# Kernel tuning notes

Measured on AMD Instinct MI355X. Metric: run time of the kernel, lower is better.

## Reference

```python
import jax, jax.numpy as jnp
import numpy as np
from jax import lax

V, T, E, H = 50000, 32, 256, 512
B, S = 64, 512


def setup_inputs() -> dict:
    key = jax.random.key(0)
    ks = jax.random.split(key, 16)
    u = lambda k, shp, s=0.05: jax.random.uniform(k, shp, jnp.float32, -s, s)
    inp = {
        'emb': jax.random.normal(ks[0], (V, E), jnp.float32) * 0.1,
        'w_ih_f': u(ks[1], (4 * H, E)), 'w_hh_f': u(ks[2], (4 * H, H)), 'b_f': u(ks[3], (4 * H,)),
        'w_ih_b': u(ks[4], (4 * H, E)), 'w_hh_b': u(ks[5], (4 * H, H)), 'b_b': u(ks[6], (4 * H,)),
        'fc_w': u(ks[7], (T, 2 * H)), 'fc_b': u(ks[8], (T,)),
        'start_trans': u(ks[9], (T,), 0.1), 'end_trans': u(ks[10], (T,), 0.1),
        'trans': u(ks[11], (T, T), 0.1),
        'x': jax.random.randint(ks[12], (B, S), 0, V),
        'tags': jax.random.randint(ks[13], (B, S), 0, T),
    }
    return inp


def _lstm_dir(xp, w_hh, reverse):
    # xp: [S, B, 4H] precomputed input projections (+ combined bias)
    b, h4 = xp.shape[1], xp.shape[2]
    h_dim = h4 // 4
    h0 = jnp.zeros((b, h_dim), xp.dtype)
    c0 = jnp.zeros((b, h_dim), xp.dtype)

    def step(carry, xt):
        h, c = carry
        gates = xt + h @ w_hh.T
        i, f, g, o = jnp.split(gates, 4, axis=-1)
        i, f, o = jax.nn.sigmoid(i), jax.nn.sigmoid(f), jax.nn.sigmoid(o)
        c = f * c + i * jnp.tanh(g)
        h = o * jnp.tanh(c)
        return (h, c), h

    _, hs = lax.scan(step, (h0, c0), xp, reverse=reverse)
    return hs  # [S, B, H]


def reference(emb, w_ih_f, w_hh_f, b_f, w_ih_b, w_hh_b, b_b, fc_w, fc_b,
              start_trans, end_trans, trans, x, tags):
    # Embedding -> [S, B, E] (time-major for the scan)
    e = jnp.transpose(emb[x], (1, 0, 2))
    # One big GEMM per direction for input projections
    xp_f = jnp.einsum('sbe,ge->sbg', e, w_ih_f) + b_f
    xp_b = jnp.einsum('sbe,ge->sbg', e, w_ih_b) + b_b
    h_f = _lstm_dir(xp_f, w_hh_f, reverse=False)
    h_b = _lstm_dir(xp_b, w_hh_b, reverse=True)
    h = jnp.concatenate([h_f, h_b], axis=-1)          # [S, B, 2H]
    em = jnp.einsum('sbh,th->sbt', h, fc_w) + fc_b     # [S, B, T] emissions

    tags_t = tags.T                                    # [S, B]
    # CRF numerator: gold path score (mask = all ones)
    emit = jnp.take_along_axis(em, tags_t[:, :, None], axis=2)[..., 0]  # [S, B]
    tr = trans[tags_t[:-1], tags_t[1:]]                                  # [S-1, B]
    num = start_trans[tags_t[0]] + emit.sum(0) + tr.sum(0) + end_trans[tags_t[-1]]

    # CRF denominator: forward algorithm (log partition)
    alpha0 = start_trans[None, :] + em[0]              # [B, T]

    def step(alpha, et):
        # alpha: [B, T_prev]; et: [B, T_next]
        nxt = jax.nn.logsumexp(alpha[:, :, None] + trans[None, :, :] + et[:, None, :], axis=1)
        return nxt, None

    alpha, _ = lax.scan(step, alpha0, em[1:])
    den = jax.nn.logsumexp(alpha + end_trans[None, :], axis=1)  # [B]

    llh = num - den
    return -jnp.mean(llh)
```

## Files before the change

### kernel.cpp

```cpp
#include <hip/hip_runtime.h>
#include <hip/hip_bf16.h>
#include <cstdint>
#include <cstddef>


typedef __attribute__((ext_vector_type(8))) short short8;
typedef __attribute__((ext_vector_type(4))) float f32x4;

__device__ __forceinline__ unsigned short f2b(float x){
  unsigned u = __float_as_uint(x);
  unsigned r = u + 0x7FFFu + ((u >> 16) & 1u);
  return (unsigned short)(r >> 16);
}
__device__ __forceinline__ float b2f(unsigned short b){
  return __uint_as_float(((unsigned)b) << 16);
}
__device__ __forceinline__ float sigf(float x){
  return 1.f / (1.f + __expf(-x));
}
__device__ __forceinline__ float tanhfast(float x){
  return 1.f - 2.f / (__expf(2.f * x) + 1.f);
}


__global__ void prep_wc_kernel(const float* __restrict__ w_ih, const float* __restrict__ w_hh,
                               unsigned short* __restrict__ wc){
  int idx = blockIdx.x * 256 + threadIdx.x;
  if(idx >= 2048 * 768) return;
  int g = idx / 768, k = idx - g * 768;
  float v = (k < 256) ? w_ih[g * 256 + k] : w_hh[g * 512 + (k - 256)];
  wc[idx] = f2b(v);
}

__global__ void prep_fcw_kernel(const float* __restrict__ fc_w, unsigned short* __restrict__ fcwN){
  int idx = blockIdx.x * 256 + threadIdx.x;
  fcwN[idx] = f2b(fc_w[idx]);
}

__global__ void gather_kernel(const float* __restrict__ emb, const int* __restrict__ x,
                              unsigned short* __restrict__ e_bf){
  int tok = blockIdx.x;
  int s = tok >> 6, b = tok & 63;
  int row = x[b * 512 + s];
  int k = threadIdx.x;
  e_bf[(size_t)tok * 256 + k] = f2b(emb[(size_t)row * 256 + k]);
}

__global__ void init_cnt_kernel(unsigned int* __restrict__ cnt){
  int idx = blockIdx.x * 256 + threadIdx.x;
  if(idx < 1024) cnt[idx] = 0;
}

__global__ __launch_bounds__(256, 1) void lstm_persist(
    const unsigned short* __restrict__ e_bf,
    const unsigned short* __restrict__ Wc_f, const unsigned short* __restrict__ Wc_b,
    const float* __restrict__ b_f, const float* __restrict__ b_b,
    unsigned short* __restrict__ st_f, unsigned short* __restrict__ st_b,
    unsigned int* __restrict__ cnt)
{
  __shared__ float gate_lds[64 * 34];

  const int tid  = threadIdx.x;
  const int wid  = tid >> 6;
  const int lane = tid & 63;
  const int dir  = blockIdx.x >> 6;
  const int slice= blockIdx.x & 63;
  const int j0   = slice * 8;

  const int mh = wid >> 1;
  const int nh = wid & 1;
  const int r0 = lane & 15;
  const int kb = (lane >> 4) * 8;

  const unsigned short* Wc   = dir ? Wc_b : Wc_f;
  const float*          bias = dir ? b_b  : b_f;
  unsigned short*       st   = dir ? st_b : st_f;
  unsigned int*         cbase= cnt + dir * 512;

  const int c = nh * 16 + r0;
  const unsigned short* wrow = Wc + (size_t)((c >> 3) * 512 + j0 + (c & 7)) * 768;
  short8 bfrag[24];
#pragma unroll
  for(int kc = 0; kc < 24; kc++)
    bfrag[kc] = *(const short8*)(wrow + kc * 32 + kb);

  const int eb = tid >> 2, jp = tid & 3;
  const float bi0 = bias[0 * 512 + j0 + 2 * jp], bi1 = bias[0 * 512 + j0 + 2 * jp + 1];
  const float bf0 = bias[1 * 512 + j0 + 2 * jp], bf1 = bias[1 * 512 + j0 + 2 * jp + 1];
  const float bg0 = bias[2 * 512 + j0 + 2 * jp], bg1 = bias[2 * 512 + j0 + 2 * jp + 1];
  const float bo0 = bias[3 * 512 + j0 + 2 * jp], bo1 = bias[3 * 512 + j0 + 2 * jp + 1];
  float cc0 = 0.f, cc1 = 0.f;

  unsigned int* st32 = (unsigned int*)st;
  const unsigned long long* stq = (const unsigned long long*)st;
  const int arow0 = mh * 32 + r0;
  const int arow1 = arow0 + 16;

  union U { unsigned long long q[2]; short8 v; };

  for(int t = 0; t < 512; t++){
    const int t_e = dir ? (511 - t) : t;

    const unsigned short* ep0 = e_bf + (size_t)t_e * 16384 + (size_t)arow0 * 256;
    const unsigned short* ep1 = e_bf + (size_t)t_e * 16384 + (size_t)arow1 * 256;
    short8 ef0[8], ef1[8];
#pragma unroll
    for(int kc = 0; kc < 8; kc++){
      ef0[kc] = *(const short8*)(ep0 + kc * 32 + kb);
      ef1[kc] = *(const short8*)(ep1 + kc * 32 + kb);
    }
    f32x4 aE0 = {0,0,0,0}, aO0 = {0,0,0,0};
    f32x4 aE1 = {0,0,0,0}, aO1 = {0,0,0,0};
#pragma unroll
    for(int kc = 0; kc < 8; kc += 2){
      aE0 = __builtin_amdgcn_mfma_f32_16x16x32_bf16(ef0[kc],   bfrag[kc],   aE0, 0,0,0);
      aE1 = __builtin_amdgcn_mfma_f32_16x16x32_bf16(ef1[kc],   bfrag[kc],   aE1, 0,0,0);
      aO0 = __builtin_amdgcn_mfma_f32_16x16x32_bf16(ef0[kc+1], bfrag[kc+1], aO0, 0,0,0);
      aO1 = __builtin_amdgcn_mfma_f32_16x16x32_bf16(ef1[kc+1], bfrag[kc+1], aO1, 0,0,0);
    }

    if(t > 0){
      const unsigned int* cp = cbase + (t - 1);
      int ok;
      do{
        unsigned v = __hip_atomic_load(cp, __ATOMIC_RELAXED, __HIP_MEMORY_SCOPE_AGENT);
        ok = __syncthreads_and((int)(v >= 64u));
      }while(!ok);
      asm volatile("" ::: "memory");

      const unsigned long long* hq0 = stq + ((size_t)(t - 1) * 8192 + (size_t)arow0 * 128 + (lane >> 4) * 2);
      const unsigned long long* hq1 = stq + ((size_t)(t - 1) * 8192 + (size_t)arow1 * 128 + (lane >> 4) * 2);
      U h0[16], h1[16];
#pragma unroll
      for(int kc = 0; kc < 16; kc++){
        h0[kc].q[0] = __hip_atomic_load(hq0 + kc * 8,     __ATOMIC_RELAXED, __HIP_MEMORY_SCOPE_AGENT);
        h0[kc].q[1] = __hip_atomic_load(hq0 + kc * 8 + 1, __ATOMIC_RELAXED, __HIP_MEMORY_SCOPE_AGENT);
      }
#pragma unroll
      for(int kc = 0; kc < 16; kc++){
        h1[kc].q[0] = __hip_atomic_load(hq1 + kc * 8,     __ATOMIC_RELAXED, __HIP_MEMORY_SCOPE_AGENT);
        h1[kc].q[1] = __hip_atomic_load(hq1 + kc * 8 + 1, __ATOMIC_RELAXED, __HIP_MEMORY_SCOPE_AGENT);
      }
#pragma unroll
      for(int kc = 0; kc < 16; kc += 2){
        aE0 = __builtin_amdgcn_mfma_f32_16x16x32_bf16(h0[kc].v,   bfrag[8+kc], aE0, 0,0,0);
        aE1 = __builtin_amdgcn_mfma_f32_16x16x32_bf16(h1[kc].v,   bfrag[8+kc], aE1, 0,0,0);
        aO0 = __builtin_amdgcn_mfma_f32_16x16x32_bf16(h0[kc+1].v, bfrag[9+kc], aO0, 0,0,0);
        aO1 = __builtin_amdgcn_mfma_f32_16x16x32_bf16(h1[kc+1].v, bfrag[9+kc], aO1, 0,0,0);
      }
    }

    f32x4 g0 = aE0 + aO0;
    f32x4 g1 = aE1 + aO1;
#pragma unroll
    for(int r = 0; r < 4; r++){
      int row = mh * 32 + (lane >> 4) * 4 + r;
      gate_lds[row * 34 + c]        = g0[r];
      gate_lds[(row + 16) * 34 + c] = g1[r];
    }
    __syncthreads();

    {
      float gi0 = gate_lds[eb * 34 + 0  + 2 * jp] + bi0, gi1 = gate_lds[eb * 34 + 1  + 2 * jp] + bi1;
      float gf0_ = gate_lds[eb * 34 + 8  + 2 * jp] + bf0, gf1_ = gate_lds[eb * 34 + 9  + 2 * jp] + bf1;
      float gg0 = gate_lds[eb * 34 + 16 + 2 * jp] + bg0, gg1 = gate_lds[eb * 34 + 17 + 2 * jp] + bg1;
      float go0 = gate_lds[eb * 34 + 24 + 2 * jp] + bo0, go1 = gate_lds[eb * 34 + 25 + 2 * jp] + bo1;
      cc0 = sigf(gf0_) * cc0 + sigf(gi0) * tanhfast(gg0);
      cc1 = sigf(gf1_) * cc1 + sigf(gi1) * tanhfast(gg1);
      float h0v = sigf(go0) * tanhfast(cc0);
      float h1v = sigf(go1) * tanhfast(cc1);
      unsigned pack = (unsigned)f2b(h0v) | ((unsigned)f2b(h1v) << 16);
      __hip_atomic_store(st32 + (size_t)t * 16384 + eb * 256 + (j0 >> 1) + jp, pack,
                         __ATOMIC_RELAXED, __HIP_MEMORY_SCOPE_AGENT);
    }
    asm volatile("s_waitcnt vmcnt(0)" ::: "memory");
    __syncthreads();
    if(tid == 0)
      __hip_atomic_fetch_add(cbase + t, 1u, __ATOMIC_RELAXED, __HIP_MEMORY_SCOPE_AGENT);
  }
}

__global__ __launch_bounds__(256) void em_kernel(
    const unsigned short* __restrict__ st_f, const unsigned short* __restrict__ st_b,
    const unsigned short* __restrict__ fcwN, const float* __restrict__ fc_b,
    float* __restrict__ em)
{
  __shared__ __align__(16) unsigned short wlds[32 * 1024];
  const int tid = threadIdx.x, wid = tid >> 6, lane = tid & 63;

#pragma unroll
  for(int i = 0; i < 16; i++){
    int vid = tid + i * 256;
    int row = vid >> 7;
    int col8 = vid & 127;
    short8 v = *(const short8*)(fcwN + (size_t)row * 1024 + col8 * 8);
    int elem = row * 1024 + ((col8 * 8) ^ ((row & 7) << 3));
    *(short8*)&wlds[elem] = v;
  }
  __syncthreads();

  const int s  = blockIdx.x * 4 + wid;
  const int r0 = lane & 15, kb = (lane >> 4) * 8;
  const unsigned short* basef = st_f + (size_t)s * 32768;
  const unsigned short* baseb = st_b + (size_t)(511 - s) * 32768;

  f32x4 acc[4][2];
#pragma unroll
  for(int m = 0; m < 4; m++){ acc[m][0] = (f32x4){0,0,0,0}; acc[m][1] = (f32x4){0,0,0,0}; }

#pragma unroll
  for(int kc = 0; kc < 32; kc++){
    const unsigned short* ab = (kc < 16) ? (basef + kc * 32 + kb)
                                         : (baseb + (kc - 16) * 32 + kb);
    int kfull = kc * 32 + kb;
    short8 b0 = *(const short8*)&wlds[(r0     ) * 1024 + (kfull ^ ((r0 & 7) << 3))];
    short8 b1 = *(const short8*)&wlds[(16 + r0) * 1024 + (kfull ^ ((r0 & 7) << 3))];
#pragma unroll
    for(int m = 0; m < 4; m++){
      short8 a = *(const short8*)(ab + (size_t)(m * 16 + r0) * 512);
      acc[m][0] = __builtin_amdgcn_mfma_f32_16x16x32_bf16(a, b0, acc[m][0], 0,0,0);
      acc[m][1] = __builtin_amdgcn_mfma_f32_16x16x32_bf16(a, b1, acc[m][1], 0,0,0);
    }
  }

  const float fb0 = fc_b[r0], fb1 = fc_b[16 + r0];
#pragma unroll
  for(int m = 0; m < 4; m++){
#pragma unroll
    for(int r = 0; r < 4; r++){
      int b = m * 16 + (lane >> 4) * 4 + r;
      em[((size_t)s * 64 + b) * 32 + r0]      = acc[m][0][r] + fb0;
      em[((size_t)s * 64 + b) * 32 + 16 + r0] = acc[m][1][r] + fb1;
    }
  }
}

__global__ __launch_bounds__(64) void crf_kernel(
    const float* __restrict__ em, const float* __restrict__ trans,
    const float* __restrict__ start_trans, const float* __restrict__ end_trans,
    const int* __restrict__ tags, float* __restrict__ llh)
{
  __shared__ float tr[32 * 33];
  __shared__ float al_s[32];
  __shared__ float red[64];
  const int b = blockIdx.x, lane = threadIdx.x;
  const int j = lane & 31, half = lane >> 5;

  for(int idx = lane; idx < 1024; idx += 64){
    int r = idx >> 5, cc = idx & 31;
    tr[r * 33 + cc] = trans[idx];
  }
  if(lane < 32) al_s[lane] = start_trans[lane] + em[(size_t)b * 32 + lane];
  __syncthreads();

  float et_next = em[((size_t)1 * 64 + b) * 32 + j];
  for(int s = 1; s < 512; s++){
    float et = et_next;
    if(s < 511) et_next = em[((size_t)(s + 1) * 64 + b) * 32 + j];
    float v[16];
    float m = -1e30f;
#pragma unroll
    for(int q = 0; q < 16; q++){
      int i = half * 16 + q;
      v[q] = al_s[i] + tr[i * 33 + j];
      m = fmaxf(m, v[q]);
    }
    float sum = 0.f;
#pragma unroll
    for(int q = 0; q < 16; q++) sum += __expf(v[q] - m);
    float mo = __shfl_xor(m, 32);
    float so = __shfl_xor(sum, 32);
    float M = fmaxf(m, mo);
    sum = sum * __expf(m - M) + so * __expf(mo - M);
    float nv = M + __logf(sum) + et;
    __syncthreads();
    if(half == 0) al_s[j] = nv;
    __syncthreads();
  }

  float den = 0.f;
  if(lane == 0){
    float m = -1e30f;
    for(int t2 = 0; t2 < 32; t2++) m = fmaxf(m, al_s[t2] + end_trans[t2]);
    float sum = 0.f;
    for(int t2 = 0; t2 < 32; t2++) sum += __expf(al_s[t2] + end_trans[t2] - m);
    den = m + __logf(sum);
  }

  float acc = 0.f;
  for(int s = lane; s < 512; s += 64){
    int tg = tags[b * 512 + s];
    acc += em[((size_t)s * 64 + b) * 32 + tg];
    if(s < 511){
      int tg2 = tags[b * 512 + s + 1];
      acc += trans[tg * 32 + tg2];
    }
  }
  red[lane] = acc;
  __syncthreads();
  if(lane == 0){
    float ns = 0.f;
    for(int i = 0; i < 64; i++) ns += red[i];
    float num = start_trans[tags[b * 512]] + ns + end_trans[tags[b * 512 + 511]];
    llh[b] = num - den;
  }
}

__global__ void final_kernel(const float* __restrict__ llh, float* __restrict__ out){
  __shared__ float red[64];
  int lane = threadIdx.x;
  red[lane] = llh[lane];
  __syncthreads();
  if(lane == 0){
    float s = 0.f;
    for(int i = 0; i < 64; i++) s += red[i];
    out[0] = -s / 64.f;
  }
}

extern "C" void kernel_launch(void* const* d_in, const int* in_sizes, int n_in,
                              void* d_out, int out_size, void* d_ws, size_t ws_size,
                              hipStream_t stream)
{
  const float* emb        = (const float*)d_in[0];
  const float* w_ih_f     = (const float*)d_in[1];
  const float* w_hh_f     = (const float*)d_in[2];
  const float* b_f        = (const float*)d_in[3];
  const float* w_ih_b     = (const float*)d_in[4];
  const float* w_hh_b     = (const float*)d_in[5];
  const float* b_b        = (const float*)d_in[6];
  const float* fc_w       = (const float*)d_in[7];
  const float* fc_b       = (const float*)d_in[8];
  const float* start_tr   = (const float*)d_in[9];
  const float* end_tr     = (const float*)d_in[10];
  const float* trans      = (const float*)d_in[11];
  const int*   x          = (const int*)d_in[12];
  const int*   tags       = (const int*)d_in[13];

  char* p = (char*)d_ws;
  unsigned short* e_bf  = (unsigned short*)p; p += (size_t)512 * 64 * 256 * 2;
  unsigned short* Wc_f  = (unsigned short*)p; p += (size_t)2048 * 768 * 2;
  unsigned short* Wc_b  = (unsigned short*)p; p += (size_t)2048 * 768 * 2;
  unsigned short* fcwN  = (unsigned short*)p; p += (size_t)32 * 1024 * 2;
  unsigned short* st_f  = (unsigned short*)p; p += (size_t)512 * 32768 * 2;
  unsigned short* st_b  = (unsigned short*)p; p += (size_t)512 * 32768 * 2;
  float*          em    = (float*)p;          p += (size_t)512 * 64 * 32 * 4;
  float*          llh   = (float*)p;          p += 256;
  unsigned int*   cnt   = (unsigned int*)p;   p += 1024 * 4;

  hipLaunchKernelGGL(prep_wc_kernel, dim3(6144), dim3(256), 0, stream, w_ih_f, w_hh_f, Wc_f);
  hipLaunchKernelGGL(prep_wc_kernel, dim3(6144), dim3(256), 0, stream, w_ih_b, w_hh_b, Wc_b);
  hipLaunchKernelGGL(prep_fcw_kernel, dim3(128), dim3(256), 0, stream, fc_w, fcwN);
  hipLaunchKernelGGL(gather_kernel, dim3(32768), dim3(256), 0, stream, emb, x, e_bf);
  hipLaunchKernelGGL(init_cnt_kernel, dim3(4), dim3(256), 0, stream, cnt);

  hipLaunchKernelGGL(lstm_persist, dim3(128), dim3(256), 0, stream,
                     e_bf, Wc_f, Wc_b, b_f, b_b, st_f, st_b, cnt);

  hipLaunchKernelGGL(em_kernel, dim3(128), dim3(256), 0, stream, st_f, st_b, fcwN, fc_b, em);
  hipLaunchKernelGGL(crf_kernel, dim3(64), dim3(64), 0, stream, em, trans, start_tr, end_tr, tags, llh);
  hipLaunchKernelGGL(final_kernel, dim3(1), dim3(64), 0, stream, llh, (float*)d_out);
}
```

Measured before the change: 6.186 ms.

## Pin each LSTM direction to one XCC and use per-slice flag sync

The persistent LSTM now launches an oversized grid. Each block reads its hardware XCC id and takes a ticket, and only the first 64 blocks on XCC 0 and on XCC 1 become workers, so each direction's recurrent exchange stays within one XCC's L2. The shared atomic counter is replaced with per-slice flags that waiting threads poll in parallel, and the hidden-state loads and stores become plain vector accesses instead of agent-scope atomics. This is meant to cut cross-die coherence latency on every timestep. The trade-offs: it relies on every worker block being resident at once, on same-L2 visibility without atomics, and on a bounded spin that could silently proceed early.

Measured after the change: 8.853 ms. +43.1%, slower.

```diff
diff --git a/kernel.cpp b/kernel.cpp
--- a/kernel.cpp
+++ b/kernel.cpp
@@ -46,27 +46,44 @@
   e_bf[(size_t)tok * 256 + k] = f2b(emb[(size_t)row * 256 + k]);
 }
 
-__global__ void init_cnt_kernel(unsigned int* __restrict__ cnt){
+__global__ void init_sync_kernel(unsigned int* __restrict__ flags,
+                                 unsigned int* __restrict__ tickets){
   int idx = blockIdx.x * 256 + threadIdx.x;
-  if(idx < 1024) cnt[idx] = 0;
-}
-
-__global__ __launch_bounds__(256, 1) void lstm_persist(
+  if(idx < 2 * 512 * 64) flags[idx] = 0;
+  if(idx < 8) tickets[idx] = 0;
+}
+
+__global__ __launch_bounds__(256, 3) void lstm_persist(
     const unsigned short* __restrict__ e_bf,
     const unsigned short* __restrict__ Wc_f, const unsigned short* __restrict__ Wc_b,
     const float* __restrict__ b_f, const float* __restrict__ b_b,
     unsigned short* __restrict__ st_f, unsigned short* __restrict__ st_b,
-    unsigned int* __restrict__ cnt)
+    unsigned int* __restrict__ flags, unsigned int* __restrict__ tickets)
 {
   __shared__ float gate_lds[64 * 34];
+  __shared__ int role_lds;
 
   const int tid  = threadIdx.x;
+
+  if(tid == 0){
+    unsigned xcc;
+    asm volatile("s_getreg_b32 %0, hwreg(HW_REG_XCC_ID)" : "=s"(xcc));
+    xcc &= 7u;
+    unsigned rank = atomicAdd(&tickets[xcc], 1u);
+    int role = -1;
+    if(xcc <= 1u && rank < 64u) role = (int)(xcc * 64u + rank);
+    role_lds = role;
+  }
+  __syncthreads();
+  const int role = role_lds;
+  if(role < 0) return;
+
+  const int dir   = role >> 6;
+  const int slice = role & 63;
+  const int j0    = slice * 8;
+
   const int wid  = tid >> 6;
   const int lane = tid & 63;
-  const int dir  = blockIdx.x >> 6;
-  const int slice= blockIdx.x & 63;
-  const int j0   = slice * 8;
-
   const int mh = wid >> 1;
   const int nh = wid & 1;
   const int r0 = lane & 15;
@@ -75,7 +92,6 @@
   const unsigned short* Wc   = dir ? Wc_b : Wc_f;
   const float*          bias = dir ? b_b  : b_f;
   unsigned short*       st   = dir ? st_b : st_f;
-  unsigned int*         cbase= cnt + dir * 512;
 
   const int c = nh * 16 + r0;
   const unsigned short* wrow = Wc + (size_t)((c >> 3) * 512 + j0 + (c & 7)) * 768;
@@ -92,11 +108,10 @@
   float cc0 = 0.f, cc1 = 0.f;
 
   unsigned int* st32 = (unsigned int*)st;
-  const unsigned long long* stq = (const unsigned long long*)st;
   const int arow0 = mh * 32 + r0;
   const int arow1 = arow0 + 16;
 
-  union U { unsigned long long q[2]; short8 v; };
+  volatile unsigned* vflags = (volatile unsigned*)flags;
 
   for(int t = 0; t < 512; t++){
     const int t_e = dir ? (511 - t) : t;
@@ -120,33 +135,28 @@
     }
 
     if(t > 0){
-      const unsigned int* cp = cbase + (t - 1);
-      int ok;
+      const volatile unsigned* fp = vflags + (((size_t)dir * 512 + (t - 1)) << 6) + (tid & 63);
+      int ok; unsigned guard = 0;
       do{
-        unsigned v = __hip_atomic_load(cp, __ATOMIC_RELAXED, __HIP_MEMORY_SCOPE_AGENT);
-        ok = __syncthreads_and((int)(v >= 64u));
-      }while(!ok);
+        unsigned v = *fp;
+        ok = __syncthreads_and((int)(v != 0u));
+      }while(!ok && (++guard < (1u << 16)));
       asm volatile("" ::: "memory");
 
-      const unsigned long long* hq0 = stq + ((size_t)(t - 1) * 8192 + (size_t)arow0 * 128 + (lane >> 4) * 2);
-      const unsigned long long* hq1 = stq + ((size_t)(t - 1) * 8192 + (size_t)arow1 * 128 + (lane >> 4) * 2);
-      U h0[16], h1[16];
+      const unsigned short* hp0 = st + (size_t)(t - 1) * 32768 + (size_t)arow0 * 512;
+      const unsigned short* hp1 = st + (size_t)(t - 1) * 32768 + (size_t)arow1 * 512;
+      short8 h0[16], h1[16];
 #pragma unroll
       for(int kc = 0; kc < 16; kc++){
-        h0[kc].q[0] = __hip_atomic_load(hq0 + kc * 8,     __ATOMIC_RELAXED, __HIP_MEMORY_SCOPE_AGENT);
-        h0[kc].q[1] = __hip_atomic_load(hq0 + kc * 8 + 1, __ATOMIC_RELAXED, __HIP_MEMORY_SCOPE_AGENT);
+        h0[kc] = *(const short8*)(hp0 + kc * 32 + kb);
+        h1[kc] = *(const short8*)(hp1 + kc * 32 + kb);
       }
 #pragma unroll
-      for(int kc = 0; kc < 16; kc++){
-        h1[kc].q[0] = __hip_atomic_load(hq1 + kc * 8,     __ATOMIC_RELAXED, __HIP_MEMORY_SCOPE_AGENT);
-        h1[kc].q[1] = __hip_atomic_load(hq1 + kc * 8 + 1, __ATOMIC_RELAXED, __HIP_MEMORY_SCOPE_AGENT);
-      }
-#pragma unroll
       for(int kc = 0; kc < 16; kc += 2){
-        aE0 = __builtin_amdgcn_mfma_f32_16x16x32_bf16(h0[kc].v,   bfrag[8+kc], aE0, 0,0,0);
-        aE1 = __builtin_amdgcn_mfma_f32_16x16x32_bf16(h1[kc].v,   bfrag[8+kc], aE1, 0,0,0);
-        aO0 = __builtin_amdgcn_mfma_f32_16x16x32_bf16(h0[kc+1].v, bfrag[9+kc], aO0, 0,0,0);
-        aO1 = __builtin_amdgcn_mfma_f32_16x16x32_bf16(h1[kc+1].v, bfrag[9+kc], aO1, 0,0,0);
+        aE0 = __builtin_amdgcn_mfma_f32_16x16x32_bf16(h0[kc],   bfrag[8+kc], aE0, 0,0,0);
+        aE1 = __builtin_amdgcn_mfma_f32_16x16x32_bf16(h1[kc],   bfrag[8+kc], aE1, 0,0,0);
+        aO0 = __builtin_amdgcn_mfma_f32_16x16x32_bf16(h0[kc+1], bfrag[9+kc], aO0, 0,0,0);
+        aO1 = __builtin_amdgcn_mfma_f32_16x16x32_bf16(h1[kc+1], bfrag[9+kc], aO1, 0,0,0);
       }
     }
 
@@ -170,13 +180,12 @@
       float h0v = sigf(go0) * tanhfast(cc0);
       float h1v = sigf(go1) * tanhfast(cc1);
       unsigned pack = (unsigned)f2b(h0v) | ((unsigned)f2b(h1v) << 16);
-      __hip_atomic_store(st32 + (size_t)t * 16384 + eb * 256 + (j0 >> 1) + jp, pack,
-                         __ATOMIC_RELAXED, __HIP_MEMORY_SCOPE_AGENT);
+      st32[(size_t)t * 16384 + eb * 256 + (j0 >> 1) + jp] = pack;
     }
     asm volatile("s_waitcnt vmcnt(0)" ::: "memory");
     __syncthreads();
     if(tid == 0)
-      __hip_atomic_fetch_add(cbase + t, 1u, __ATOMIC_RELAXED, __HIP_MEMORY_SCOPE_AGENT);
+      vflags[(((size_t)dir * 512 + t) << 6) + slice] = 1u;
   }
 }
 
@@ -346,16 +355,17 @@
   unsigned short* st_b  = (unsigned short*)p; p += (size_t)512 * 32768 * 2;
   float*          em    = (float*)p;          p += (size_t)512 * 64 * 32 * 4;
   float*          llh   = (float*)p;          p += 256;
-  unsigned int*   cnt   = (unsigned int*)p;   p += 1024 * 4;
+  unsigned int*   flags = (unsigned int*)p;   p += (size_t)2 * 512 * 64 * 4;
+  unsigned int*   tickets=(unsigned int*)p;   p += 64;
 
   hipLaunchKernelGGL(prep_wc_kernel, dim3(6144), dim3(256), 0, stream, w_ih_f, w_hh_f, Wc_f);
   hipLaunchKernelGGL(prep_wc_kernel, dim3(6144), dim3(256), 0, stream, w_ih_b, w_hh_b, Wc_b);
   hipLaunchKernelGGL(prep_fcw_kernel, dim3(128), dim3(256), 0, stream, fc_w, fcwN);
   hipLaunchKernelGGL(gather_kernel, dim3(32768), dim3(256), 0, stream, emb, x, e_bf);
-  hipLaunchKernelGGL(init_cnt_kernel, dim3(4), dim3(256), 0, stream, cnt);
-
-  hipLaunchKernelGGL(lstm_persist, dim3(128), dim3(256), 0, stream,
-                     e_bf, Wc_f, Wc_b, b_f, b_b, st_f, st_b, cnt);
+  hipLaunchKernelGGL(init_sync_kernel, dim3(258), dim3(256), 0, stream, flags, tickets);
+
+  hipLaunchKernelGGL(lstm_persist, dim3(768), dim3(256), 0, stream,
+                     e_bf, Wc_f, Wc_b, b_f, b_b, st_f, st_b, flags, tickets);
 
   hipLaunchKernelGGL(em_kernel, dim3(128), dim3(256), 0, stream, st_f, st_b, fcwN, fc_b, em);
   hipLaunchKernelGGL(crf_kernel, dim3(64), dim3(64), 0, stream, em, trans, start_tr, end_tr, tags, llh);
```
